# Kernel optimization log

Hardware: AMD Instinct MI355X
Metric: run time of the kernel (lower is better)

## Reference

```python
import jax, jax.numpy as jnp
import numpy as np

B, T, C, V = 4, 2048, 1024, 50257


def setup_inputs() -> dict:
    key = jax.random.key(0)
    k1, k2, k3 = jax.random.split(key, 3)
    x = jax.random.normal(k1, (B, T, C), dtype=jnp.float32)
    y = jax.random.randint(k2, (B, T), 0, V, dtype=jnp.int64)
    # nn.Linear(C, V): weight [V, C], bias [V]
    W = jax.random.normal(k3, (V, C), dtype=jnp.float32) * (1.0 / np.sqrt(C))
    b = jnp.zeros((V,), dtype=jnp.float32)
    return {"x": x, "y": y, "W": W, "b": b}


def reference(x, y, W, b):
    # logits: [B*T, V]
    logits = jnp.einsum("btc,vc->btv", x, W).reshape(B * T, V) + b
    labels = y.reshape(-1)  # [B*T]
    logp = jax.nn.log_softmax(logits, axis=-1)
    nll = -jnp.take_along_axis(logp, labels[:, None], axis=-1)[:, 0]
    return jnp.mean(nll)
```

## Files before the change

kernel.cpp:

```cpp
#include <hip/hip_runtime.h>


#define M_TOT 8192
#define K_TOT 1024
#define V_TOT 50257
#define NT    393
#define NPAD  (NT * 128)
#define PSTRIDE (NT * 2)
#define KB    (K_TOT / 64)

typedef __attribute__((ext_vector_type(8)))  int   int8v;
typedef __attribute__((ext_vector_type(16))) float floatx16;

__device__ __forceinline__ int f4_to_fp8x4(float4 v) {
  int r = __builtin_amdgcn_cvt_pk_fp8_f32(v.x, v.y, 0, false);
  r = __builtin_amdgcn_cvt_pk_fp8_f32(v.z, v.w, r, true);
  return r;
}

__global__ __launch_bounds__(256) void pack_kernel(
    const float* __restrict__ src, char* __restrict__ dst, int nrows) {
  int t = blockIdx.x * 256 + threadIdx.x;
  int lane = t & 63;
  int kb   = (t >> 6) & (KB - 1);
  int g    = t >> 10;
  int srow = g * 32 + (lane & 31);
  int k0   = kb * 64 + (lane >> 5) * 32;
  int8v out = {};
  if (srow < nrows) {
    const float4* s = (const float4*)(src + (long)srow * K_TOT + k0);
#pragma unroll
    for (int j = 0; j < 8; ++j) out[j] = f4_to_fp8x4(s[j]);
  }
  *(int8v*)(dst + (long)t * 32) = out;
}

__global__ __launch_bounds__(256, 3) void gemm_lse_kernel(
    const char* __restrict__ pW, const char* __restrict__ pX,
    const float* __restrict__ bias, float* __restrict__ psum) {
  const int tid  = threadIdx.x;
  const int wave = tid >> 6;
  const int lane = tid & 63;
  const int wv   = wave >> 1;
  const int wb   = wave & 1;
  const int mblk = blockIdx.x;
  const int vblk = blockIdx.y;

  const long GSTRIDE = (long)KB * 64 * 32;
  const char* pa0 = pW + (long)(vblk * 4 + wv * 2) * GSTRIDE + (long)lane * 32;
  const char* pa1 = pa0 + GSTRIDE;
  const char* pb0 = pX + (long)(mblk * 4 + wb * 2) * GSTRIDE + (long)lane * 32;
  const char* pb1 = pb0 + GSTRIDE;

  floatx16 acc[2][2] = {};
#pragma unroll 2
  for (int kb = 0; kb < KB; ++kb) {
    const int off = kb * 2048;
    int8v a0 = *(const int8v*)(pa0 + off);
    int8v a1 = *(const int8v*)(pa1 + off);
    int8v b0 = *(const int8v*)(pb0 + off);
    int8v b1 = *(const int8v*)(pb1 + off);
    acc[0][0] = __builtin_amdgcn_mfma_scale_f32_32x32x64_f8f6f4(
        a0, b0, acc[0][0], 0, 0, 0, 0x7F7F7F7F, 0, 0x7F7F7F7F);
    acc[0][1] = __builtin_amdgcn_mfma_scale_f32_32x32x64_f8f6f4(
        a0, b1, acc[0][1], 0, 0, 0, 0x7F7F7F7F, 0, 0x7F7F7F7F);
    acc[1][0] = __builtin_amdgcn_mfma_scale_f32_32x32x64_f8f6f4(
        a1, b0, acc[1][0], 0, 0, 0, 0x7F7F7F7F, 0, 0x7F7F7F7F);
    acc[1][1] = __builtin_amdgcn_mfma_scale_f32_32x32x64_f8f6f4(
        a1, b1, acc[1][1], 0, 0, 0, 0x7F7F7F7F, 0, 0x7F7F7F7F);
  }

  const int half = lane >> 5, l32 = lane & 31;
  const int vbase = vblk * 128 + wv * 64 + 4 * half;
  float s0 = 0.0f, s1 = 0.0f;
#pragma unroll
  for (int tv = 0; tv < 2; ++tv) {
#pragma unroll
    for (int reg = 0; reg < 16; ++reg) {
      int v = vbase + tv * 32 + (reg & 3) + 8 * (reg >> 2);
      float bv = (v < V_TOT) ? bias[v] : -1e30f;
      s0 += __expf(acc[tv][0][reg] + bv);
      s1 += __expf(acc[tv][1][reg] + bv);
    }
  }
  s0 += __shfl_xor(s0, 32, 64);
  s1 += __shfl_xor(s1, 32, 64);
  if (half == 0) {
    int m = mblk * 128 + wb * 64 + l32;
    long base = (long)m * PSTRIDE + vblk * 2 + wv;
    psum[base] = s0;
    psum[base + (long)32 * PSTRIDE] = s1;
  }
}

__global__ __launch_bounds__(256) void finalize_kernel(
    const float* __restrict__ psum, const float* __restrict__ x,
    const float* __restrict__ W, const float* __restrict__ b,
    const int* __restrict__ y, float* __restrict__ loss) {
  const int wave = threadIdx.x >> 6;
  const int lane = threadIdx.x & 63;
  const int r = blockIdx.x * 4 + wave;

  const float* ps = psum + (long)r * PSTRIDE;
  float s = 0.0f;
  for (int j = lane; j < PSTRIDE; j += 64) s += ps[j];
#pragma unroll
  for (int o = 1; o < 64; o <<= 1) s += __shfl_xor(s, o, 64);

  int label = y[r];
  const float4* xr = (const float4*)(x + (long)r * K_TOT);
  const float4* wr = (const float4*)(W + (long)label * K_TOT);
  float d = 0.0f;
  for (int j = lane; j < K_TOT / 4; j += 64) {
    float4 a = xr[j], w = wr[j];
    d += a.x * w.x + a.y * w.y + a.z * w.z + a.w * w.w;
  }
#pragma unroll
  for (int o = 1; o < 64; o <<= 1) d += __shfl_xor(d, o, 64);

  if (lane == 0) loss[r] = logf(s) - d - b[label];
}

__global__ __launch_bounds__(256) void reduce_kernel(
    const float* __restrict__ loss, float* __restrict__ out) {
  const int tid = threadIdx.x;
  float s = 0.0f;
  for (int j = tid; j < M_TOT; j += 256) s += loss[j];
#pragma unroll
  for (int o = 1; o < 64; o <<= 1) s += __shfl_xor(s, o, 64);
  __shared__ float wsum[4];
  if ((tid & 63) == 0) wsum[tid >> 6] = s;
  __syncthreads();
  if (tid == 0)
    out[0] = (wsum[0] + wsum[1] + wsum[2] + wsum[3]) * (1.0f / (float)M_TOT);
}

extern "C" void kernel_launch(void* const* d_in, const int* in_sizes, int n_in,
                              void* d_out, int out_size, void* d_ws, size_t ws_size,
                              hipStream_t stream) {
  (void)in_sizes; (void)n_in; (void)out_size; (void)ws_size;
  const float* x = (const float*)d_in[0];
  const int*   y = (const int*)d_in[1];
  const float* W = (const float*)d_in[2];
  const float* b = (const float*)d_in[3];
  float* out = (float*)d_out;

  char* ws = (char*)d_ws;
  const size_t PX_BYTES = (size_t)M_TOT * K_TOT;
  const size_t PW_BYTES = (size_t)NPAD * K_TOT;
  const size_t PS_BYTES = (size_t)M_TOT * PSTRIDE * 4;
  char*  pX   = ws;
  char*  pW   = ws + PX_BYTES;
  float* psum = (float*)(ws + PX_BYTES + PW_BYTES);
  float* loss = (float*)(ws + PX_BYTES + PW_BYTES + PS_BYTES);

  pack_kernel<<<(M_TOT / 32) * KB * 64 / 256, 256, 0, stream>>>(x, pX, M_TOT);
  pack_kernel<<<(NPAD / 32) * KB * 64 / 256, 256, 0, stream>>>(W, pW, V_TOT);
  gemm_lse_kernel<<<dim3(M_TOT / 128, NT), 256, 0, stream>>>(pW, pX, b, psum);
  finalize_kernel<<<M_TOT / 4, 256, 0, stream>>>(psum, x, W, b, y, loss);
  reduce_kernel<<<1, 256, 0, stream>>>(loss, out);
}
```

Baseline: 795.5 us.

## Enlarge GEMM vocab tile to 256 and coalesce fp8 pack loads

Each wave now computes a 4x2 grid of 32x32 MFMA tiles instead of 2x2, so the block covers 256 vocab rows and the X fragments are reused across twice as many W fragments, cutting global load traffic per MFMA. The vocab grid dimension halves and the partial-sum stride shrinks, so the finalize kernel has fewer partials to add. The pack kernel is reorganised so consecutive threads read contiguous 32-byte chunks of a row and scatter 8-byte stores into the same fragment layout, replacing the earlier strided per-thread float4 reads. The trade-off is more accumulator registers, with occupancy lowered from 3 to 2 blocks per CU, and more vocabulary padding (50432 rows instead of 50304).

```diff
diff --git a/kernel.cpp b/kernel.cpp
--- a/kernel.cpp
+++ b/kernel.cpp
@@ -4,10 +4,11 @@
 #define M_TOT 8192
 #define K_TOT 1024
 #define V_TOT 50257
-#define NT    393
-#define NPAD  (NT * 128)
-#define PSTRIDE (NT * 2)
+#define NVB   197
+#define NPAD  (NVB * 256)
+#define PSTRIDE (NVB * 2)
 #define KB    (K_TOT / 64)
+#define GSTRIDE ((long)KB * 64 * 32)
 
 typedef __attribute__((ext_vector_type(8)))  int   int8v;
 typedef __attribute__((ext_vector_type(16))) float floatx16;
@@ -20,22 +21,22 @@
 
 __global__ __launch_bounds__(256) void pack_kernel(
     const float* __restrict__ src, char* __restrict__ dst, int nrows) {
-  int t = blockIdx.x * 256 + threadIdx.x;
-  int lane = t & 63;
-  int kb   = (t >> 6) & (KB - 1);
-  int g    = t >> 10;
-  int srow = g * 32 + (lane & 31);
-  int k0   = kb * 64 + (lane >> 5) * 32;
-  int8v out = {};
+  const int kb = blockIdx.x, g = blockIdx.y;
+  const int i = threadIdx.x;
+  const int r = i >> 3, seg = i & 7;
+  const int srow = g * 32 + r;
+  int lo = 0, hi = 0;
   if (srow < nrows) {
-    const float4* s = (const float4*)(src + (long)srow * K_TOT + k0);
-#pragma unroll
-    for (int j = 0; j < 8; ++j) out[j] = f4_to_fp8x4(s[j]);
+    const float4* s = (const float4*)(src + (long)srow * K_TOT + kb * 64 + seg * 8);
+    lo = f4_to_fp8x4(s[0]);
+    hi = f4_to_fp8x4(s[1]);
   }
-  *(int8v*)(dst + (long)t * 32) = out;
+  const int h = seg >> 2;
+  char* d = dst + (((long)(g * KB + kb) * 64 + h * 32 + r) * 32 + (seg & 3) * 8);
+  *(int2*)d = make_int2(lo, hi);
 }
 
-__global__ __launch_bounds__(256, 3) void gemm_lse_kernel(
+__global__ __launch_bounds__(256, 2) void gemm_lse_kernel(
     const char* __restrict__ pW, const char* __restrict__ pX,
     const float* __restrict__ bias, float* __restrict__ psum) {
   const int tid  = threadIdx.x;
@@ -46,35 +47,37 @@
   const int mblk = blockIdx.x;
   const int vblk = blockIdx.y;
 
-  const long GSTRIDE = (long)KB * 64 * 32;
-  const char* pa0 = pW + (long)(vblk * 4 + wv * 2) * GSTRIDE + (long)lane * 32;
-  const char* pa1 = pa0 + GSTRIDE;
-  const char* pb0 = pX + (long)(mblk * 4 + wb * 2) * GSTRIDE + (long)lane * 32;
-  const char* pb1 = pb0 + GSTRIDE;
+  const char* pa[4];
+  const char* pb[2];
+#pragma unroll
+  for (int tv = 0; tv < 4; ++tv)
+    pa[tv] = pW + (long)(vblk * 8 + wv * 4 + tv) * GSTRIDE + (long)lane * 32;
+#pragma unroll
+  for (int tn = 0; tn < 2; ++tn)
+    pb[tn] = pX + (long)(mblk * 4 + wb * 2 + tn) * GSTRIDE + (long)lane * 32;
 
-  floatx16 acc[2][2] = {};
+  floatx16 acc[4][2] = {};
 #pragma unroll 2
   for (int kb = 0; kb < KB; ++kb) {
     const int off = kb * 2048;
-    int8v a0 = *(const int8v*)(pa0 + off);
-    int8v a1 = *(const int8v*)(pa1 + off);
-    int8v b0 = *(const int8v*)(pb0 + off);
-    int8v b1 = *(const int8v*)(pb1 + off);
-    acc[0][0] = __builtin_amdgcn_mfma_scale_f32_32x32x64_f8f6f4(
-        a0, b0, acc[0][0], 0, 0, 0, 0x7F7F7F7F, 0, 0x7F7F7F7F);
-    acc[0][1] = __builtin_amdgcn_mfma_scale_f32_32x32x64_f8f6f4(
-        a0, b1, acc[0][1], 0, 0, 0, 0x7F7F7F7F, 0, 0x7F7F7F7F);
-    acc[1][0] = __builtin_amdgcn_mfma_scale_f32_32x32x64_f8f6f4(
-        a1, b0, acc[1][0], 0, 0, 0, 0x7F7F7F7F, 0, 0x7F7F7F7F);
-    acc[1][1] = __builtin_amdgcn_mfma_scale_f32_32x32x64_f8f6f4(
-        a1, b1, acc[1][1], 0, 0, 0, 0x7F7F7F7F, 0, 0x7F7F7F7F);
+    int8v a[4], b[2];
+#pragma unroll
+    for (int tn = 0; tn < 2; ++tn) b[tn] = *(const int8v*)(pb[tn] + off);
+#pragma unroll
+    for (int tv = 0; tv < 4; ++tv) a[tv] = *(const int8v*)(pa[tv] + off);
+#pragma unroll
+    for (int tv = 0; tv < 4; ++tv)
+#pragma unroll
+      for (int tn = 0; tn < 2; ++tn)
+        acc[tv][tn] = __builtin_amdgcn_mfma_scale_f32_32x32x64_f8f6f4(
+            a[tv], b[tn], acc[tv][tn], 0, 0, 0, 0x7F7F7F7F, 0, 0x7F7F7F7F);
   }
 
   const int half = lane >> 5, l32 = lane & 31;
-  const int vbase = vblk * 128 + wv * 64 + 4 * half;
+  const int vbase = vblk * 256 + wv * 128 + 4 * half;
   float s0 = 0.0f, s1 = 0.0f;
 #pragma unroll
-  for (int tv = 0; tv < 2; ++tv) {
+  for (int tv = 0; tv < 4; ++tv) {
 #pragma unroll
     for (int reg = 0; reg < 16; ++reg) {
       int v = vbase + tv * 32 + (reg & 3) + 8 * (reg >> 2);
@@ -154,9 +157,9 @@
   float* psum = (float*)(ws + PX_BYTES + PW_BYTES);
   float* loss = (float*)(ws + PX_BYTES + PW_BYTES + PS_BYTES);
 
-  pack_kernel<<<(M_TOT / 32) * KB * 64 / 256, 256, 0, stream>>>(x, pX, M_TOT);
-  pack_kernel<<<(NPAD / 32) * KB * 64 / 256, 256, 0, stream>>>(W, pW, V_TOT);
-  gemm_lse_kernel<<<dim3(M_TOT / 128, NT), 256, 0, stream>>>(pW, pX, b, psum);
+  pack_kernel<<<dim3(KB, M_TOT / 32), 256, 0, stream>>>(x, pX, M_TOT);
+  pack_kernel<<<dim3(KB, NPAD / 32), 256, 0, stream>>>(W, pW, V_TOT);
+  gemm_lse_kernel<<<dim3(M_TOT / 128, NVB), 256, 0, stream>>>(pW, pX, b, psum);
   finalize_kernel<<<M_TOT / 4, 256, 0, stream>>>(psum, x, W, b, y, loss);
   reduce_kernel<<<1, 256, 0, stream>>>(loss, out);
 }
```

Result: faster. 729.9 us (-8.2%).
